# Performance work log

Hardware: AMD Instinct MI355X
Metric: run time of the kernel (lower is better)

Reference implementation:

```python
import jax, jax.numpy as jnp
import numpy as np

C = 256; Ca = C // 2; WH = 8; WW = 8; K = 3; NH = 8; HD = Ca // NH
EPS_LN = 1e-5; EPS_BN = 1e-5

def _rel_pos_idx(wh, ww):
    coords = np.stack(np.meshgrid(np.arange(wh), np.arange(ww), indexing='ij'))  # (2,wh,ww)
    flat = coords.reshape(2, -1)
    rel = (flat[:, :, None] - flat[:, None, :]).transpose(1, 2, 0).astype(np.int64)  # (N,N,2)
    rel[..., 0] += wh - 1
    rel[..., 1] += ww - 1
    rel[..., 0] *= 2 * ww - 1
    return jnp.asarray(rel.sum(-1))  # (N,N)

REL_IDX = _rel_pos_idx(WH, WW)

def _ln(x, g, b):
    m = x.mean(-1, keepdims=True)
    v = x.var(-1, keepdims=True)
    return (x - m) / jnp.sqrt(v + EPS_LN) * g + b

def _bn(x, g, b):  # eval-mode BN, running_mean=0, running_var=1; x is NCHW
    return x * (g / np.sqrt(1.0 + EPS_BN))[None, :, None, None] + b[None, :, None, None]

def _conv1x1(x, w, b):  # w: (O, I)
    return jnp.einsum('bchw,oc->bohw', x, w) + b[None, :, None, None]

def _rwp(x, h, w, wh, ww):  # windows (B*nW, wh*ww, c) -> image (B, c, h, w)
    Bn, N, c = x.shape
    nh, nw = h // wh, w // ww
    B = Bn // (nh * nw)
    x = x.reshape(B, nh, nw, wh, ww, c)
    return x.transpose(0, 5, 1, 3, 2, 4).reshape(B, c, h, w)

def _wp(x, wh, ww):  # image (B, c, h, w) -> windows (B*nW, wh*ww, c)
    B, c, h, w = x.shape
    x = x.reshape(B, c, h // wh, wh, w // ww, ww)
    return x.transpose(0, 2, 4, 3, 5, 1).reshape(-1, wh * ww, c)

def _gelu(t):
    return jax.nn.gelu(t, approximate=False)

def forward(x, rel_pos_bias, attn_w, attn_b, attn_ln_g, attn_ln_b,
            conv_w, conv_b, conv_bn_g, conv_bn_b,
            ci_w1, ci_b1, ci_bn_g, ci_bn_b, ci_w2, ci_b2,
            pr_w, pr_b, cn_bn_g, cn_bn_b,
            qkv_w, qkv_b,
            si_w1, si_b1, si_bn_g, si_bn_b, si_w2, si_b2,
            an_g, an_b, out_w, out_b, h, w):
    B_, N, Cfull = x.shape
    x_attn = _ln(x @ attn_w + attn_b, attn_ln_g, attn_ln_b)  # (B_, N, Ca)
    # conv branch -- note: source applies RWP to raw x (proj_cnn output is dead code)
    x_img = _rwp(x, h, w, WH, WW)  # (B, C, h, w)
    pad = K // 2
    x_cnn = jax.lax.conv_general_dilated(
        x_img, conv_w, (1, 1), [(pad, pad), (pad, pad)],
        dimension_numbers=('NCHW', 'OIHW', 'NCHW'), feature_group_count=Cfull)
    x_cnn = _gelu(_bn(x_cnn + conv_b[None, :, None, None], conv_bn_g, conv_bn_b))
    gap = x_cnn.mean((2, 3), keepdims=True)  # (B, C, 1, 1)
    ci = _conv1x1(gap, ci_w1, ci_b1)
    ci = _gelu(_bn(ci, ci_bn_g, ci_bn_b))
    ci = _conv1x1(ci, ci_w2, ci_b2)  # (B, Ca, 1, 1)
    x_cnn = _conv1x1(x_cnn, pr_w, pr_b)  # (B, Ca, h, w)
    # windowed attention
    qkv = (x_attn @ qkv_w + qkv_b).reshape(B_, N, 3, NH, HD).transpose(2, 0, 3, 1, 4)
    q, k, v = qkv[0], qkv[1], qkv[2]  # each (B_, NH, N, HD)
    B = ci.shape[0]
    ci_s = jax.nn.sigmoid(ci).reshape(B, 1, NH, 1, HD)
    v = (v.reshape(B, B_ // B, NH, N, HD) * ci_s).reshape(B_, NH, N, HD)
    scale = HD ** -0.5
    attn = jnp.einsum('bhnd,bhmd->bhnm', q * scale, k)
    bias = rel_pos_bias[REL_IDX]  # (N, N, NH)
    attn = jax.nn.softmax(attn + bias.transpose(2, 0, 1)[None], axis=-1)
    x_attn = jnp.einsum('bhnm,bhmd->bhnd', attn, v).transpose(0, 2, 1, 3).reshape(B_, N, Ca)
    # spatial interaction gating of conv branch
    x_sp = _rwp(x_attn, h, w, WH, WW)  # (B, Ca, h, w)
    si = _conv1x1(x_sp, si_w1, si_b1)
    si = _gelu(_bn(si, si_bn_g, si_bn_b))
    si = _conv1x1(si, si_w2, si_b2)  # (B, 1, h, w)
    x_cnn = jax.nn.sigmoid(si * x_cnn)
    x_cnn = _bn(x_cnn, cn_bn_g, cn_bn_b)
    x_cnn = _wp(x_cnn, WH, WW)  # (B_, N, Ca)
    x_attn = _ln(x_attn, an_g, an_b)
    return jnp.concatenate([x_attn, x_cnn], axis=-1) @ out_w + out_b

def setup_inputs() -> dict:
    key = jax.random.key(0)
    ks = jax.random.split(key, 12)
    B_, N = 2048, WH * WW
    s = 0.02
    return dict(
        x=jax.random.normal(ks[0], (B_, N, C), jnp.float32),
        rel_pos_bias=jax.random.uniform(ks[1], ((2 * WH - 1) * (2 * WW - 1), NH), jnp.float32),
        attn_w=jax.random.normal(ks[2], (C, Ca)) * s, attn_b=jnp.zeros((Ca,)),
        attn_ln_g=jnp.ones((Ca,)), attn_ln_b=jnp.zeros((Ca,)),
        conv_w=jax.random.normal(ks[3], (C, 1, K, K)) * s, conv_b=jnp.zeros((C,)),
        conv_bn_g=jnp.ones((C,)), conv_bn_b=jnp.zeros((C,)),
        ci_w1=jax.random.normal(ks[4], (C // 8, C)) * s, ci_b1=jnp.zeros((C // 8,)),
        ci_bn_g=jnp.ones((C // 8,)), ci_bn_b=jnp.zeros((C // 8,)),
        ci_w2=jax.random.normal(ks[5], (Ca, C // 8)) * s, ci_b2=jnp.zeros((Ca,)),
        pr_w=jax.random.normal(ks[6], (Ca, C)) * s, pr_b=jnp.zeros((Ca,)),
        cn_bn_g=jnp.ones((Ca,)), cn_bn_b=jnp.zeros((Ca,)),
        qkv_w=jax.random.normal(ks[7], (Ca, 3 * Ca)) * s, qkv_b=jnp.zeros((3 * Ca,)),
        si_w1=jax.random.normal(ks[8], (C // 16, Ca)) * s, si_b1=jnp.zeros((C // 16,)),
        si_bn_g=jnp.ones((C // 16,)), si_bn_b=jnp.zeros((C // 16,)),
        si_w2=jax.random.normal(ks[9], (1, C // 16)) * s, si_b2=jnp.zeros((1,)),
        an_g=jnp.ones((Ca,)), an_b=jnp.zeros((Ca,)),
        out_w=jax.random.normal(ks[10], (C, C)) * s, out_b=jnp.zeros((C,)),
        h=64, w=64,
    )

def reference(x, rel_pos_bias, attn_w, attn_b, attn_ln_g, attn_ln_b,
              conv_w, conv_b, conv_bn_g, conv_bn_b,
              ci_w1, ci_b1, ci_bn_g, ci_bn_b, ci_w2, ci_b2,
              pr_w, pr_b, cn_bn_g, cn_bn_b,
              qkv_w, qkv_b,
              si_w1, si_b1, si_bn_g, si_bn_b, si_w2, si_b2,
              an_g, an_b, out_w, out_b, h, w):
    return forward(x, rel_pos_bias, attn_w, attn_b, attn_ln_g, attn_ln_b,
                   conv_w, conv_b, conv_bn_g, conv_bn_b,
                   ci_w1, ci_b1, ci_bn_g, ci_bn_b, ci_w2, ci_b2,
                   pr_w, pr_b, cn_bn_g, cn_bn_b,
                   qkv_w, qkv_b,
                   si_w1, si_b1, si_bn_g, si_bn_b, si_w2, si_b2,
                   an_g, an_b, out_w, out_b, h, w)
```

## Files before the change

### kernel.cpp

```cpp
#include <hip/hip_runtime.h>
#include <math.h>


#define BNR 0.9999950000374998f

typedef __attribute__((ext_vector_type(8))) short short8;
typedef __attribute__((ext_vector_type(4))) float f32x4;
typedef __attribute__((ext_vector_type(4))) _Float16 half4;
typedef __attribute__((ext_vector_type(8))) _Float16 half8;
typedef __attribute__((ext_vector_type(2))) _Float16 h2v;

__device__ __forceinline__ float gelu_f(float x) {
  const float z = x * (1.0f + 0.044715f * x * x);
  return x / (1.0f + __expf(-1.5957691216057308f * z));
}
__device__ __forceinline__ unsigned short f2bf(float f) {
  unsigned int u = __builtin_bit_cast(unsigned int, f);
  u += 0x7fffu + ((u >> 16) & 1u);
  return (unsigned short)(u >> 16);
}
__device__ __forceinline__ float bf2f(unsigned short h) {
  unsigned int u = ((unsigned int)h) << 16;
  return __builtin_bit_cast(float, u);
}
__device__ __forceinline__ void ld8(const unsigned short* p, float* o) {
  const short8 v = *(const short8*)p;
#pragma unroll
  for (int i = 0; i < 8; ++i) o[i] = bf2f((unsigned short)v[i]);
}
__device__ __forceinline__ unsigned int pkh(float a, float b) {
  return __builtin_bit_cast(unsigned int, __builtin_amdgcn_cvt_pkrtz(a, b));
}

#define ATI(r, ch) (((r) << 8) + ((((ch) ^ ((r)&7))) << 3))

__global__ __launch_bounds__(256) void kpack(
    const float* __restrict__ aw, const float* __restrict__ qw,
    const float* __restrict__ prw, const float* __restrict__ ow,
    const float* __restrict__ sw1, unsigned short* __restrict__ awp,
    unsigned short* __restrict__ qwp, unsigned short* __restrict__ prwp,
    unsigned short* __restrict__ owp, unsigned short* __restrict__ sw1p) {
  const int b = blockIdx.x;
  const float* src; unsigned short* dst; int fs, K, N, NT, trans, f16o;
  if (b < 64)       { fs = b;       src = aw;  dst = awp;  K = 256; N = 128; NT = 8;  trans = 0; f16o = 0; }
  else if (b < 160) { fs = b - 64;  src = qw;  dst = qwp;  K = 128; N = 384; NT = 24; trans = 0; f16o = 0; }
  else if (b < 224) { fs = b - 160; src = prw; dst = prwp; K = 256; N = 128; NT = 8;  trans = 1; f16o = 1; }
  else if (b < 352) { fs = b - 224; src = ow;  dst = owp;  K = 256; N = 256; NT = 16; trans = 0; f16o = 0; }
  else              { fs = b - 352; src = sw1; dst = sw1p; K = 128; N = 16;  NT = 1;  trans = 1; f16o = 0; }
  const int ks = fs / NT, nt = fs % NT;
  for (int idx = threadIdx.x; idx < 512; idx += 256) {
    const int l = idx >> 3, i = idx & 7;
    const int k = ks * 32 + ((l >> 4) << 3) + i, n = nt * 16 + (l & 15);
    const float v = trans ? src[n * K + k] : src[k * N + n];
    dst[(fs * 64 + l) * 8 + i] =
        f16o ? __builtin_bit_cast(unsigned short, (_Float16)v) : f2bf(v);
  }
}

__global__ __launch_bounds__(256) void kbias(const float* __restrict__ rpb,
                                             unsigned short* __restrict__ bt) {
  const int i = blockIdx.x * 256 + threadIdx.x;
  const int h = i >> 12, n = (i >> 6) & 63, m = i & 63;
  const int ny = n >> 3, nx = n & 7, my = m >> 3, mx = m & 7;
  const float v = rpb[((ny - my + 7) * 15 + (nx - mx + 7)) * 8 + h];
  bt[i] = __builtin_bit_cast(unsigned short, (_Float16)v);
}

__global__ __launch_bounds__(256) void k1_attn_ln(
    const float* __restrict__ x, const unsigned short* __restrict__ awp,
    const float* __restrict__ ab, const float* __restrict__ lg,
    const float* __restrict__ lb, unsigned short* __restrict__ xattn,
    unsigned short* __restrict__ xb) {
  const int tid = threadIdx.x, w = tid >> 6, l = tid & 63;
  const int lr = l & 15, lg4 = l >> 4;
  const int r0 = blockIdx.x * 64 + w * 16;
  const float* xp = x + (size_t)(r0 + lr) * 256 + lg4 * 8;
  unsigned short* xbp = xb + (size_t)(r0 + lr) * 256 + lg4 * 8;
  short8 a[8];
#pragma unroll
  for (int ks = 0; ks < 8; ++ks) {
    const float4 f0 = *(const float4*)(xp + ks * 32);
    const float4 f1 = *(const float4*)(xp + ks * 32 + 4);
    short8 av;
    av[0] = f2bf(f0.x); av[1] = f2bf(f0.y); av[2] = f2bf(f0.z); av[3] = f2bf(f0.w);
    av[4] = f2bf(f1.x); av[5] = f2bf(f1.y); av[6] = f2bf(f1.z); av[7] = f2bf(f1.w);
    a[ks] = av;
    uint4 hv;
    hv.x = pkh(f0.x, f0.y); hv.y = pkh(f0.z, f0.w);
    hv.z = pkh(f1.x, f1.y); hv.w = pkh(f1.z, f1.w);
    *(uint4*)(xbp + ks * 32) = hv;
  }
  f32x4 acc[8];
#pragma unroll
  for (int nt = 0; nt < 8; ++nt) acc[nt] = (f32x4)0.f;
#pragma unroll
  for (int nt = 0; nt < 8; ++nt)
#pragma unroll
    for (int ks = 0; ks < 8; ++ks) {
      const short8 bfr = *(const short8*)(awp + ((ks * 8 + nt) * 64 + l) * 8);
      acc[nt] = __builtin_amdgcn_mfma_f32_16x16x32_bf16(a[ks], bfr, acc[nt], 0, 0, 0);
    }
  float bias[8], gam[8], bet[8];
#pragma unroll
  for (int nt = 0; nt < 8; ++nt) {
    const int col = nt * 16 + lr;
    bias[nt] = ab[col]; gam[nt] = lg[col]; bet[nt] = lb[col];
  }
#pragma unroll
  for (int j = 0; j < 4; ++j) {
    float s = 0.f, qq = 0.f;
#pragma unroll
    for (int nt = 0; nt < 8; ++nt) {
      const float v = acc[nt][j] + bias[nt];
      acc[nt][j] = v; s += v; qq += v * v;
    }
    s += __shfl_xor(s, 1); s += __shfl_xor(s, 2);
    s += __shfl_xor(s, 4); s += __shfl_xor(s, 8);
    qq += __shfl_xor(qq, 1); qq += __shfl_xor(qq, 2);
    qq += __shfl_xor(qq, 4); qq += __shfl_xor(qq, 8);
    const float mean = s * (1.f / 128.f);
    const float var = qq * (1.f / 128.f) - mean * mean;
    const float rstd = rsqrtf(var + 1e-5f);
    const int row = r0 + lg4 * 4 + j;
#pragma unroll
    for (int nt = 0; nt < 8; ++nt)
      xattn[(size_t)row * 128 + nt * 16 + lr] =
          f2bf((acc[nt][j] - mean) * rstd * gam[nt] + bet[nt]);
  }
}

__global__ __launch_bounds__(256) void k25_conv(
    const unsigned short* __restrict__ xb, const float* __restrict__ cw,
    const float* __restrict__ cb, const float* __restrict__ bg,
    const float* __restrict__ bb, const unsigned short* __restrict__ prwp,
    const float* __restrict__ prb, unsigned short* __restrict__ xpr,
    float* __restrict__ gpart) {
  __shared__ unsigned short gl[32][264];
  const int tid = threadIdx.x;
  const int bid = (blockIdx.x & 7) * 512 + (blockIdx.x >> 3);
  const int b = bid >> 7;
  const int y = (bid >> 1) & 63;
  const int xt = (bid & 1) * 32;
  const int w = tid >> 6, l = tid & 63;
  {
    const int c0 = l << 2;
    h2v w01[9], w23[9];
#pragma unroll
    for (int k = 0; k < 9; ++k) {
      w01[k][0] = (_Float16)cw[(c0 + 0) * 9 + k];
      w01[k][1] = (_Float16)cw[(c0 + 1) * 9 + k];
      w23[k][0] = (_Float16)cw[(c0 + 2) * 9 + k];
      w23[k][1] = (_Float16)cw[(c0 + 3) * 9 + k];
    }
    const float4 cbf = *(const float4*)&cb[c0];
    float4 scf = *(const float4*)&bg[c0];
    scf.x *= BNR; scf.y *= BNR; scf.z *= BNR; scf.w *= BNR;
    const float4 sbf = *(const float4*)&bb[c0];
    h2v cb01 = {(_Float16)cbf.x, (_Float16)cbf.y};
    h2v cb23 = {(_Float16)cbf.z, (_Float16)cbf.w};
    h2v sc01 = {(_Float16)scf.x, (_Float16)scf.y};
    h2v sc23 = {(_Float16)scf.z, (_Float16)scf.w};
    h2v sb01 = {(_Float16)sbf.x, (_Float16)sbf.y};
    h2v sb23 = {(_Float16)sbf.z, (_Float16)sbf.w};
    float4 gsum = make_float4(0.f, 0.f, 0.f, 0.f);
    const int px0 = xt + w * 8;
#pragma unroll
    for (int sc2 = 0; sc2 < 2; ++sc2) {
      const int p0 = px0 + sc2 * 4;
      h2v v0[3][6], v1[3][6];
#pragma unroll
      for (int dy = 0; dy < 3; ++dy) {
        const int yy = y + dy - 1;
        const bool vy = (unsigned)yy < 64u;
        const int ybase = vy ? ((b * 64 + (yy >> 3) * 8) * 64 + (yy & 7) * 8) : 0;
#pragma unroll
        for (int q = 0; q < 6; ++q) {
          const int xx = p0 - 1 + q;
          h2v a = (h2v)(_Float16)0.f, c = (h2v)(_Float16)0.f;
          if (vy && (unsigned)xx < 64u) {
            const int row = ybase + (xx >> 3) * 64 + (xx & 7);
            const uint2 u = *(const uint2*)&xb[(size_t)row * 256 + c0];
            a = __builtin_bit_cast(h2v, u.x);
            c = __builtin_bit_cast(h2v, u.y);
          }
          v0[dy][q] = a; v1[dy][q] = c;
        }
      }
#pragma unroll
      for (int p = 0; p < 4; ++p) {
        h2v s0 = cb01, s1 = cb23;
#pragma unroll
        for (int dy = 0; dy < 3; ++dy)
#pragma unroll
          for (int dx = 0; dx < 3; ++dx) {
            s0 = w01[dy * 3 + dx] * v0[dy][p + dx] + s0;
            s1 = w23[dy * 3 + dx] * v1[dy][p + dx] + s1;
          }
        s0 = s0 * sc01 + sb01;
        s1 = s1 * sc23 + sb23;
        const float g0 = gelu_f((float)s0[0]), g1 = gelu_f((float)s0[1]);
        const float g2 = gelu_f((float)s1[0]), g3 = gelu_f((float)s1[1]);
        uint2 pk;
        pk.x = pkh(g0, g1); pk.y = pkh(g2, g3);
        *(uint2*)&gl[w * 8 + sc2 * 4 + p][c0] = pk;
        gsum.x += g0; gsum.y += g1; gsum.z += g2; gsum.w += g3;
      }
    }
    *(float4*)&gpart[(size_t)bid * 256 + c0] = gsum;
  }
  __syncthreads();
  const int lr = l & 15, lg4 = l >> 4;
  const int mr0 = (w & 1) * 16, nt0 = (w >> 1) * 4;
  half8 a[8];
#pragma unroll
  for (int ks = 0; ks < 8; ++ks)
    a[ks] = __builtin_bit_cast(half8,
                               *(const short8*)&gl[mr0 + lr][ks * 32 + lg4 * 8]);
  f32x4 acc[4];
#pragma unroll
  for (int nt = 0; nt < 4; ++nt) acc[nt] = (f32x4)0.f;
#pragma unroll
  for (int nt = 0; nt < 4; ++nt)
#pragma unroll
    for (int ks = 0; ks < 8; ++ks) {
      const half8 bfr = __builtin_bit_cast(
          half8, *(const short8*)(prwp + ((ks * 8 + nt0 + nt) * 64 + l) * 8));
      acc[nt] = __builtin_amdgcn_mfma_f32_16x16x32_f16(a[ks], bfr, acc[nt], 0, 0, 0);
    }
#pragma unroll
  for (int nt = 0; nt < 4; ++nt) {
    const int col = (nt0 + nt) * 16 + lr;
    const float bv = prb[col];
#pragma unroll
    for (int j = 0; j < 4; ++j) {
      const int pix = (b * 64 + y) * 64 + xt + mr0 + lg4 * 4 + j;
      xpr[(size_t)pix * 128 + col] = f2bf(acc[nt][j] + bv);
    }
  }
}

__global__ __launch_bounds__(128) void k3_ci(
    const float* __restrict__ gp, const float* __restrict__ w1,
    const float* __restrict__ b1, const float* __restrict__ g1,
    const float* __restrict__ bb1, const float* __restrict__ w2,
    const float* __restrict__ b2, float* __restrict__ cis) {
  __shared__ float gm[256];
  __shared__ float c1[32];
  const int b = blockIdx.x, tid = threadIdx.x;
  for (int c = tid; c < 256; c += 128) {
    float s = 0.f;
    for (int p = 0; p < 128; ++p) s += gp[(size_t)(b * 128 + p) * 256 + c];
    gm[c] = s * (1.f / 4096.f);
  }
  __syncthreads();
  if (tid < 32) {
    float s = b1[tid];
    for (int c = 0; c < 256; ++c) s = fmaf(gm[c], w1[tid * 256 + c], s);
    s = s * (g1[tid] * BNR) + bb1[tid];
    c1[tid] = gelu_f(s);
  }
  __syncthreads();
  float s = b2[tid];
#pragma unroll
  for (int i = 0; i < 32; ++i) s = fmaf(c1[i], w2[tid * 32 + i], s);
  cis[b * 128 + tid] = 1.f / (1.f + __expf(-s));
}

__global__ __launch_bounds__(256) void k4_attn(
    const unsigned short* __restrict__ xa, const unsigned short* __restrict__ qwp,
    const float* __restrict__ qb, const float* __restrict__ cis,
    const unsigned short* __restrict__ biasT, unsigned short* __restrict__ attn) {
  __shared__ _Float16 QS[4][64][36];
  __shared__ _Float16 KS[4][64][36];
  __shared__ _Float16 VTS[4][32][68];
  const int tid = threadIdx.x;
  const int win = blockIdx.x, img = win >> 6;
  const int w = tid >> 6, l = tid & 63, lr = l & 15, lg4 = l >> 4;
  int ntg6[6];
#pragma unroll
  for (int nt6 = 0; nt6 < 6; ++nt6)
    ntg6[nt6] = (nt6 < 2) ? 2 * w + nt6 : (nt6 < 4) ? 6 + 2 * w + nt6
                                                    : 12 + 2 * w + nt6;
  float qbv[6];
#pragma unroll
  for (int nt6 = 0; nt6 < 6; ++nt6) qbv[nt6] = qb[ntg6[nt6] * 16 + lr];
  float cisv[2];
#pragma unroll
  for (int t = 0; t < 2; ++t) cisv[t] = cis[img * 128 + w * 32 + t * 16 + lr];
  f32x4 acc[4][6];
#pragma unroll
  for (int mt = 0; mt < 4; ++mt)
#pragma unroll
    for (int nt6 = 0; nt6 < 6; ++nt6) acc[mt][nt6] = (f32x4)0.f;
#pragma unroll
  for (int ks = 0; ks < 4; ++ks) {
    short8 a[4];
#pragma unroll
    for (int mt = 0; mt < 4; ++mt)
      a[mt] = *(const short8*)(xa + (size_t)(win * 64 + mt * 16 + lr) * 128 +
                               ks * 32 + lg4 * 8);
#pragma unroll
    for (int nt6 = 0; nt6 < 6; ++nt6) {
      const short8 bfr =
          *(const short8*)(qwp + ((ks * 24 + ntg6[nt6]) * 64 + l) * 8);
#pragma unroll
      for (int mt = 0; mt < 4; ++mt)
        acc[mt][nt6] = __builtin_amdgcn_mfma_f32_16x16x32_bf16(a[mt], bfr,
                                                               acc[mt][nt6], 0, 0, 0);
    }
  }
#pragma unroll
  for (int mt = 0; mt < 4; ++mt)
#pragma unroll
    for (int nt6 = 0; nt6 < 6; ++nt6)
#pragma unroll
      for (int j = 0; j < 4; ++j) {
        const int row = mt * 16 + lg4 * 4 + j;
        const float v = acc[mt][nt6][j] + qbv[nt6];
        if (nt6 < 2) QS[w][row][nt6 * 16 + lr] = (_Float16)(v * 0.25f);
        else if (nt6 < 4) KS[w][row][(nt6 - 2) * 16 + lr] = (_Float16)v;
        else VTS[w][(nt6 - 4) * 16 + lr][row] = (_Float16)(v * cisv[nt6 - 4]);
      }
  for (int hi = 0; hi < 2; ++hi) {
    const int h = w * 2 + hi;
    half4 aK[4], bQ[4], bV[4];
#pragma unroll
    for (int mt = 0; mt < 4; ++mt)
      aK[mt] = *(const half4*)&KS[w][mt * 16 + lr][hi * 16 + lg4 * 4];
#pragma unroll
    for (int nt = 0; nt < 4; ++nt)
      bQ[nt] = *(const half4*)&QS[w][nt * 16 + lr][hi * 16 + lg4 * 4];
#pragma unroll
    for (int kt = 0; kt < 4; ++kt)
      bV[kt] = *(const half4*)&VTS[w][hi * 16 + lr][kt * 16 + lg4 * 4];
    f32x4 s[4][4];
#pragma unroll
    for (int mt = 0; mt < 4; ++mt)
#pragma unroll
      for (int nt = 0; nt < 4; ++nt)
        s[mt][nt] = __builtin_amdgcn_mfma_f32_16x16x16f16(aK[mt], bQ[nt],
                                                          (f32x4)0.f, 0, 0, 0);
#pragma unroll
    for (int nt = 0; nt < 4; ++nt) {
      const int n = nt * 16 + lr;
      const unsigned short* bp = biasT + (((h << 6) + n) << 6);
#pragma unroll
      for (int mt = 0; mt < 4; ++mt) {
        const half4 b4 = *(const half4*)(bp + mt * 16 + lg4 * 4);
        s[mt][nt][0] += (float)b4[0];
        s[mt][nt][1] += (float)b4[1];
        s[mt][nt][2] += (float)b4[2];
        s[mt][nt][3] += (float)b4[3];
      }
    }
    float inv[4];
#pragma unroll
    for (int nt = 0; nt < 4; ++nt) {
      float m0 = -1e30f;
#pragma unroll
      for (int mt = 0; mt < 4; ++mt)
#pragma unroll
        for (int r = 0; r < 4; ++r) m0 = fmaxf(m0, s[mt][nt][r]);
      m0 = fmaxf(m0, __shfl_xor(m0, 16));
      m0 = fmaxf(m0, __shfl_xor(m0, 32));
      float d0 = 0.f;
#pragma unroll
      for (int mt = 0; mt < 4; ++mt)
#pragma unroll
        for (int r = 0; r < 4; ++r) {
          const float e = __expf(s[mt][nt][r] - m0);
          s[mt][nt][r] = e;
          d0 += e;
        }
      d0 += __shfl_xor(d0, 16);
      d0 += __shfl_xor(d0, 32);
      inv[nt] = 1.f / d0;
    }
    half4 pa[4][4];
#pragma unroll
    for (int nt = 0; nt < 4; ++nt)
#pragma unroll
      for (int kt = 0; kt < 4; ++kt) {
        half4 p;
#pragma unroll
        for (int r = 0; r < 4; ++r) p[r] = (_Float16)(s[kt][nt][r] * inv[nt]);
        pa[nt][kt] = p;
      }
    f32x4 o[4];
#pragma unroll
    for (int nt = 0; nt < 4; ++nt) o[nt] = (f32x4)0.f;
#pragma unroll
    for (int nt = 0; nt < 4; ++nt)
#pragma unroll
      for (int kt = 0; kt < 4; ++kt)
        o[nt] = __builtin_amdgcn_mfma_f32_16x16x16f16(pa[nt][kt], bV[kt], o[nt], 0, 0, 0);
#pragma unroll
    for (int nt = 0; nt < 4; ++nt)
#pragma unroll
      for (int r = 0; r < 4; ++r) {
        const int token = win * 64 + nt * 16 + lg4 * 4 + r;
        attn[(size_t)token * 128 + h * 16 + lr] = f2bf(o[nt][r]);
      }
  }
}

__global__ __launch_bounds__(256) void k6_tail(
    const unsigned short* __restrict__ attn, const unsigned short* __restrict__ xpr,
    const unsigned short* __restrict__ sw1p, const float* __restrict__ sb1,
    const float* __restrict__ sgc, const float* __restrict__ sbc,
    const float* __restrict__ sw2, const float* __restrict__ sb2,
    const float* __restrict__ cg, const float* __restrict__ cbb,
    const float* __restrict__ ag, const float* __restrict__ abb,
    const unsigned short* __restrict__ owp, const float* __restrict__ ob,
    float* __restrict__ out) {
  __shared__ unsigned short At[64 * 256];
  __shared__ float sifl[64];
  __shared__ float statl[64][2];
  const int tid = threadIdx.x;
  const int R0 = blockIdx.x * 64;
  const int w = tid >> 6, l = tid & 63, lr = l & 15, lg4 = l >> 4;
  for (int i = tid; i < 1024; i += 256) {
    const int r = i >> 4, c16 = i & 15;
    *(uint4*)&At[ATI(r, c16)] =
        *(const uint4*)&attn[(size_t)(R0 + r) * 128 + c16 * 8];
    const int R = R0 + r, win = R >> 6, tt = R & 63;
    const int bimg = win >> 6, wy = (win >> 3) & 7, wx = win & 7;
    const int pix = (bimg * 64 + wy * 8 + (tt >> 3)) * 64 + wx * 8 + (tt & 7);
    *(uint4*)&At[ATI(r, 16 + c16)] =
        *(const uint4*)&xpr[(size_t)pix * 128 + c16 * 8];
  }
  __syncthreads();
  {
    const int r = tid >> 2, q = tid & 3;
    float xv[32];
#pragma unroll
    for (int b8 = 0; b8 < 4; ++b8) ld8(&At[ATI(r, q * 4 + b8)], xv + b8 * 8);
    float ps = 0.f, pq = 0.f;
#pragma unroll
    for (int j = 0; j < 32; ++j) { ps += xv[j]; pq += xv[j] * xv[j]; }
    ps += __shfl_xor(ps, 1); ps += __shfl_xor(ps, 2);
    pq += __shfl_xor(pq, 1); pq += __shfl_xor(pq, 2);
    if (q == 0) {
      const float mean = ps * (1.f / 128.f);
      const float var = pq * (1.f / 128.f) - mean * mean;
      statl[r][0] = mean;
      statl[r][1] = rsqrtf(var + 1e-5f);
    }
  }
  {
    const int row = w * 16 + lr;
    f32x4 sa = (f32x4)0.f;
#pragma unroll
    for (int ks = 0; ks < 4; ++ks) {
      const short8 a4 = *(const short8*)&At[ATI(row, ks * 4 + lg4)];
      const short8 bfr = *(const short8*)(sw1p + (ks * 64 + l) * 8);
      sa = __builtin_amdgcn_mfma_f32_16x16x32_bf16(a4, bfr, sa, 0, 0, 0);
    }
    const float sb1v = sb1[lr], g1v = sgc[lr] * BNR, b1v = sbc[lr];
    const float w2v = sw2[lr], sb2v = sb2[0];
#pragma unroll
    for (int j = 0; j < 4; ++j) {
      float s = (sa[j] + sb1v) * g1v + b1v;
      float p = gelu_f(s) * w2v;
      p += __shfl_xor(p, 1); p += __shfl_xor(p, 2);
      p += __shfl_xor(p, 4); p += __shfl_xor(p, 8);
      if (lr == 0) sifl[w * 16 + lg4 * 4 + j] = p + sb2v;
    }
  }
  __syncthreads();
  {
    const int c = tid & 127;
    const float agv = ag[c], abbv = abb[c];
    const float cgv = cg[c] * BNR, cbbv = cbb[c];
#pragma unroll
    for (int k = 0; k < 32; ++k) {
      const int r = (tid >> 7) + k * 2;
      const int ia = ATI(r, c >> 3) + (c & 7);
      const int ic = ATI(r, 16 + (c >> 3)) + (c & 7);
      float a = bf2f(At[ia]);
      a = (a - statl[r][0]) * statl[r][1] * agv + abbv;
      At[ia] = f2bf(a);
      const float cv = bf2f(At[ic]);
      const float g = 1.f / (1.f + __expf(-sifl[r] * cv));
      At[ic] = f2bf(g * cgv + cbbv);
    }
  }
  __syncthreads();
  const int row = w * 16 + lr;
  short8 a[8];
#pragma unroll
  for (int ks = 0; ks < 8; ++ks)
    a[ks] = *(const short8*)&At[ATI(row, ks * 4 + lg4)];
  f32x4 acc[16];
#pragma unroll
  for (int nt = 0; nt < 16; ++nt) acc[nt] = (f32x4)0.f;
#pragma unroll
  for (int nt = 0; nt < 16; ++nt)
#pragma unroll
    for (int ks = 0; ks < 8; ++ks) {
      const short8 bfr = *(const short8*)(owp + ((ks * 16 + nt) * 64 + l) * 8);
      acc[nt] = __builtin_amdgcn_mfma_f32_16x16x32_bf16(a[ks], bfr, acc[nt], 0, 0, 0);
    }
#pragma unroll
  for (int nt = 0; nt < 16; ++nt) {
    const int col = nt * 16 + lr;
    const float bv = ob[col];
#pragma unroll
    for (int j = 0; j < 4; ++j)
      out[(size_t)(R0 + w * 16 + lg4 * 4 + j) * 256 + col] = acc[nt][j] + bv;
  }
}

extern "C" void kernel_launch(void* const* d_in, const int* in_sizes, int n_in,
                              void* d_out, int out_size, void* d_ws,
                              size_t ws_size, hipStream_t stream) {
  (void)in_sizes; (void)n_in; (void)out_size; (void)ws_size;
  const float* x      = (const float*)d_in[0];
  const float* rpb    = (const float*)d_in[1];
  const float* attn_w = (const float*)d_in[2];
  const float* attn_b = (const float*)d_in[3];
  const float* aln_g  = (const float*)d_in[4];
  const float* aln_b  = (const float*)d_in[5];
  const float* conv_w = (const float*)d_in[6];
  const float* conv_b = (const float*)d_in[7];
  const float* cbn_g  = (const float*)d_in[8];
  const float* cbn_b  = (const float*)d_in[9];
  const float* ci_w1  = (const float*)d_in[10];
  const float* ci_b1  = (const float*)d_in[11];
  const float* ci_bg  = (const float*)d_in[12];
  const float* ci_bb  = (const float*)d_in[13];
  const float* ci_w2  = (const float*)d_in[14];
  const float* ci_b2  = (const float*)d_in[15];
  const float* pr_w   = (const float*)d_in[16];
  const float* pr_b   = (const float*)d_in[17];
  const float* cn_g   = (const float*)d_in[18];
  const float* cn_b   = (const float*)d_in[19];
  const float* qkv_w  = (const float*)d_in[20];
  const float* qkv_b  = (const float*)d_in[21];
  const float* si_w1  = (const float*)d_in[22];
  const float* si_b1  = (const float*)d_in[23];
  const float* si_bg  = (const float*)d_in[24];
  const float* si_bb  = (const float*)d_in[25];
  const float* si_w2  = (const float*)d_in[26];
  const float* si_b2  = (const float*)d_in[27];
  const float* an_g   = (const float*)d_in[28];
  const float* an_b   = (const float*)d_in[29];
  const float* out_w  = (const float*)d_in[30];
  const float* out_b  = (const float*)d_in[31];

  unsigned short* xb    = (unsigned short*)d_ws;
  unsigned short* xattn = xb + 33554432;
  unsigned short* attn  = xattn + 16777216;
  unsigned short* xpr   = attn + 16777216;
  float* gpart = (float*)(xpr + 16777216);
  float* cis   = gpart + 1048576;
  unsigned short* awp   = (unsigned short*)(cis + 4096);
  unsigned short* qwp   = awp + 32768;
  unsigned short* prwp  = qwp + 49152;
  unsigned short* owp   = prwp + 32768;
  unsigned short* sw1p  = owp + 65536;
  unsigned short* biasT = sw1p + 2048;

  kpack<<<356, 256, 0, stream>>>(attn_w, qkv_w, pr_w, out_w, si_w1,
                                 awp, qwp, prwp, owp, sw1p);
  kbias<<<128, 256, 0, stream>>>(rpb, biasT);
  k1_attn_ln<<<2048, 256, 0, stream>>>(x, awp, attn_b, aln_g, aln_b, xattn, xb);
  k25_conv<<<4096, 256, 0, stream>>>(xb, conv_w, conv_b, cbn_g, cbn_b, prwp,
                                     pr_b, xpr, gpart);
  k3_ci<<<32, 128, 0, stream>>>(gpart, ci_w1, ci_b1, ci_bg, ci_bb, ci_w2,
                                ci_b2, cis);
  k4_attn<<<2048, 256, 0, stream>>>(xattn, qwp, qkv_b, cis, biasT, attn);
  k6_tail<<<2048, 256, 0, stream>>>(attn, xpr, sw1p, si_b1, si_bg, si_bb,
                                    si_w2, si_b2, cn_g, cn_b, an_g, an_b,
                                    owp, out_b, (float*)d_out);
}
```

Before: 313.6 us.

## Split QKV projection in attention kernel and keep V in registers

The attention kernel's QKV projection is split into two phases. Q/K are computed first and written to padded LDS, then V is computed separately and kept directly in registers in MFMA B-operand layout, which removes the transposed VTS shared buffer. The change also adds a launch_bounds occupancy hint of 4 and changes the LDS row pitch. It aims to cut LDS usage and peak accumulator registers to raise occupancy, at the cost of reloading the xa activation fragments twice.

New measurement: 300.2 us. -4.3%, faster.

```diff
diff --git a/kernel.cpp b/kernel.cpp
--- a/kernel.cpp
+++ b/kernel.cpp
@@ -266,73 +266,106 @@
   cis[b * 128 + tid] = 1.f / (1.f + __expf(-s));
 }
 
-__global__ __launch_bounds__(256) void k4_attn(
+__global__ __launch_bounds__(256, 4) void k4_attn(
     const unsigned short* __restrict__ xa, const unsigned short* __restrict__ qwp,
     const float* __restrict__ qb, const float* __restrict__ cis,
     const unsigned short* __restrict__ biasT, unsigned short* __restrict__ attn) {
-  __shared__ _Float16 QS[4][64][36];
-  __shared__ _Float16 KS[4][64][36];
-  __shared__ _Float16 VTS[4][32][68];
+  __shared__ _Float16 QS[4][64][38];
+  __shared__ _Float16 KS[4][64][38];
   const int tid = threadIdx.x;
   const int win = blockIdx.x, img = win >> 6;
   const int w = tid >> 6, l = tid & 63, lr = l & 15, lg4 = l >> 4;
-  int ntg6[6];
-#pragma unroll
-  for (int nt6 = 0; nt6 < 6; ++nt6)
-    ntg6[nt6] = (nt6 < 2) ? 2 * w + nt6 : (nt6 < 4) ? 6 + 2 * w + nt6
-                                                    : 12 + 2 * w + nt6;
-  float qbv[6];
-#pragma unroll
-  for (int nt6 = 0; nt6 < 6; ++nt6) qbv[nt6] = qb[ntg6[nt6] * 16 + lr];
-  float cisv[2];
-#pragma unroll
-  for (int t = 0; t < 2; ++t) cisv[t] = cis[img * 128 + w * 32 + t * 16 + lr];
-  f32x4 acc[4][6];
-#pragma unroll
-  for (int mt = 0; mt < 4; ++mt)
-#pragma unroll
-    for (int nt6 = 0; nt6 < 6; ++nt6) acc[mt][nt6] = (f32x4)0.f;
-#pragma unroll
-  for (int ks = 0; ks < 4; ++ks) {
-    short8 a[4];
+  {
+    float qbv[4];
+#pragma unroll
+    for (int t = 0; t < 4; ++t) {
+      const int gnt = (t < 2) ? (2 * w + t) : (8 + 2 * w + t - 2);
+      qbv[t] = qb[gnt * 16 + lr];
+    }
+    f32x4 acc[4][4];
 #pragma unroll
     for (int mt = 0; mt < 4; ++mt)
-      a[mt] = *(const short8*)(xa + (size_t)(win * 64 + mt * 16 + lr) * 128 +
-                               ks * 32 + lg4 * 8);
-#pragma unroll
-    for (int nt6 = 0; nt6 < 6; ++nt6) {
-      const short8 bfr =
-          *(const short8*)(qwp + ((ks * 24 + ntg6[nt6]) * 64 + l) * 8);
+#pragma unroll
+      for (int t = 0; t < 4; ++t) acc[mt][t] = (f32x4)0.f;
+#pragma unroll
+    for (int ks = 0; ks < 4; ++ks) {
+      short8 a[4];
 #pragma unroll
       for (int mt = 0; mt < 4; ++mt)
-        acc[mt][nt6] = __builtin_amdgcn_mfma_f32_16x16x32_bf16(a[mt], bfr,
-                                                               acc[mt][nt6], 0, 0, 0);
-    }
-  }
-#pragma unroll
-  for (int mt = 0; mt < 4; ++mt)
-#pragma unroll
-    for (int nt6 = 0; nt6 < 6; ++nt6)
-#pragma unroll
-      for (int j = 0; j < 4; ++j) {
-        const int row = mt * 16 + lg4 * 4 + j;
-        const float v = acc[mt][nt6][j] + qbv[nt6];
-        if (nt6 < 2) QS[w][row][nt6 * 16 + lr] = (_Float16)(v * 0.25f);
-        else if (nt6 < 4) KS[w][row][(nt6 - 2) * 16 + lr] = (_Float16)v;
-        else VTS[w][(nt6 - 4) * 16 + lr][row] = (_Float16)(v * cisv[nt6 - 4]);
-      }
+        a[mt] = *(const short8*)(xa + (size_t)(win * 64 + mt * 16 + lr) * 128 +
+                                 ks * 32 + lg4 * 8);
+#pragma unroll
+      for (int t = 0; t < 4; ++t) {
+        const int gnt = (t < 2) ? (2 * w + t) : (8 + 2 * w + t - 2);
+        const short8 bfr = *(const short8*)(qwp + ((ks * 24 + gnt) * 64 + l) * 8);
+#pragma unroll
+        for (int mt = 0; mt < 4; ++mt)
+          acc[mt][t] = __builtin_amdgcn_mfma_f32_16x16x32_bf16(a[mt], bfr,
+                                                               acc[mt][t], 0, 0, 0);
+      }
+    }
+#pragma unroll
+    for (int mt = 0; mt < 4; ++mt)
+#pragma unroll
+      for (int t = 0; t < 4; ++t)
+#pragma unroll
+        for (int j = 0; j < 4; ++j) {
+          const int row = mt * 16 + lg4 * 4 + j;
+          const float v = acc[mt][t][j] + qbv[t];
+          if (t < 2) QS[w][row][t * 16 + lr] = (_Float16)(v * 0.25f);
+          else KS[w][row][(t - 2) * 16 + lr] = (_Float16)v;
+        }
+  }
+  half4 bV2[2][4];
+  {
+    float qbv[2], cisv[2];
+#pragma unroll
+    for (int t = 0; t < 2; ++t) {
+      qbv[t] = qb[(16 + 2 * w + t) * 16 + lr];
+      cisv[t] = cis[img * 128 + (2 * w + t) * 16 + lr];
+    }
+    f32x4 accv[4][2];
+#pragma unroll
+    for (int mt = 0; mt < 4; ++mt)
+#pragma unroll
+      for (int t = 0; t < 2; ++t) accv[mt][t] = (f32x4)0.f;
+#pragma unroll
+    for (int ks = 0; ks < 4; ++ks) {
+      short8 a[4];
+#pragma unroll
+      for (int mt = 0; mt < 4; ++mt)
+        a[mt] = *(const short8*)(xa + (size_t)(win * 64 + mt * 16 + lr) * 128 +
+                                 ks * 32 + lg4 * 8);
+#pragma unroll
+      for (int t = 0; t < 2; ++t) {
+        const short8 bfr =
+            *(const short8*)(qwp + ((ks * 24 + 16 + 2 * w + t) * 64 + l) * 8);
+#pragma unroll
+        for (int mt = 0; mt < 4; ++mt)
+          accv[mt][t] = __builtin_amdgcn_mfma_f32_16x16x32_bf16(a[mt], bfr,
+                                                                accv[mt][t], 0, 0, 0);
+      }
+    }
+#pragma unroll
+    for (int t = 0; t < 2; ++t)
+#pragma unroll
+      for (int kt = 0; kt < 4; ++kt) {
+        half4 p;
+#pragma unroll
+        for (int i = 0; i < 4; ++i)
+          p[i] = (_Float16)((accv[kt][t][i] + qbv[t]) * cisv[t]);
+        bV2[t][kt] = p;
+      }
+  }
   for (int hi = 0; hi < 2; ++hi) {
     const int h = w * 2 + hi;
-    half4 aK[4], bQ[4], bV[4];
+    half4 aK[4], bQ[4];
 #pragma unroll
     for (int mt = 0; mt < 4; ++mt)
       aK[mt] = *(const half4*)&KS[w][mt * 16 + lr][hi * 16 + lg4 * 4];
 #pragma unroll
     for (int nt = 0; nt < 4; ++nt)
       bQ[nt] = *(const half4*)&QS[w][nt * 16 + lr][hi * 16 + lg4 * 4];
-#pragma unroll
-    for (int kt = 0; kt < 4; ++kt)
-      bV[kt] = *(const half4*)&VTS[w][hi * 16 + lr][kt * 16 + lg4 * 4];
     f32x4 s[4][4];
 #pragma unroll
     for (int mt = 0; mt < 4; ++mt)
@@ -393,7 +426,8 @@
     for (int nt = 0; nt < 4; ++nt)
 #pragma unroll
       for (int kt = 0; kt < 4; ++kt)
-        o[nt] = __builtin_amdgcn_mfma_f32_16x16x16f16(pa[nt][kt], bV[kt], o[nt], 0, 0, 0);
+        o[nt] = __builtin_amdgcn_mfma_f32_16x16x16f16(pa[nt][kt], bV2[hi][kt],
+                                                      o[nt], 0, 0, 0);
 #pragma unroll
     for (int nt = 0; nt < 4; ++nt)
 #pragma unroll
```
